# Performance work log

Measured on AMD Instinct MI355X. Metric: run time of the kernel, lower is better.

## Reference

```python
import jax, jax.numpy as jnp
import numpy as np

N_NODES = 50000
N_EDGES = 600000
IN_CH = 300
HID = 128
N_CLASSES = 2
N_GRAPHS = 128
BN_EPS = 1e-5


def setup_inputs() -> dict:
    key = jax.random.key(0)
    ks = jax.random.split(key, 24)
    x = jax.random.normal(ks[0], (N_NODES, IN_CH), dtype=jnp.float32)
    edge_index = jax.random.randint(ks[1], (2, N_EDGES), 0, N_NODES, dtype=jnp.int64)
    batch = jnp.sort(jax.random.randint(ks[2], (N_NODES,), 0, N_GRAPHS, dtype=jnp.int64))

    def glorot(k, shape):
        fan_in, fan_out = shape
        s = jnp.sqrt(2.0 / (fan_in + fan_out)).astype(jnp.float32)
        return jax.random.normal(k, shape, dtype=jnp.float32) * s

    inp = {"x": x, "edge_index": edge_index, "batch": batch}
    # SAGEConv params: W_l (neighbor branch), W_r (root branch), bias
    dims = [(IN_CH, HID), (HID, HID), (HID, HID)]
    for i, (din, dout) in enumerate(dims, start=1):
        inp[f"W{i}l"] = glorot(ks[3 * i], (din, dout))
        inp[f"W{i}r"] = glorot(ks[3 * i + 1], (din, dout))
        inp[f"b{i}"] = jnp.zeros((dout,), dtype=jnp.float32)
        inp[f"g{i}"] = jnp.ones((dout,), dtype=jnp.float32)   # BN gamma
        inp[f"be{i}"] = jnp.zeros((dout,), dtype=jnp.float32)  # BN beta
    inp["Wc"] = glorot(ks[20], (HID, N_CLASSES))
    inp["bc"] = jnp.zeros((N_CLASSES,), dtype=jnp.float32)
    return inp


def _sage_conv(x, src, dst, Wl, Wr, b):
    # mean-aggregate neighbor features (messages flow src -> dst)
    msg_sum = jax.ops.segment_sum(x[src], dst, num_segments=N_NODES)
    deg = jax.ops.segment_sum(jnp.ones((src.shape[0],), dtype=x.dtype), dst,
                              num_segments=N_NODES)
    mean = msg_sum / jnp.maximum(deg, 1.0)[:, None]
    return mean @ Wl + x @ Wr + b


def _bn_relu(h, gamma, beta):
    mu = jnp.mean(h, axis=0)
    var = jnp.var(h, axis=0)
    h = (h - mu) * jax.lax.rsqrt(var + BN_EPS) * gamma + beta
    return jax.nn.relu(h)


def reference(x, edge_index, batch,
              W1l, W1r, b1, g1, be1,
              W2l, W2r, b2, g2, be2,
              W3l, W3r, b3, g3, be3,
              Wc, bc):
    src, dst = edge_index[0], edge_index[1]
    h = _bn_relu(_sage_conv(x, src, dst, W1l, W1r, b1), g1, be1)
    h = _bn_relu(_sage_conv(h, src, dst, W2l, W2r, b2), g2, be2)
    h = _bn_relu(_sage_conv(h, src, dst, W3l, W3r, b3), g3, be3)
    # global mean pool per graph
    pooled = jax.ops.segment_sum(h, batch, num_segments=N_GRAPHS)
    cnt = jax.ops.segment_sum(jnp.ones((h.shape[0],), dtype=h.dtype), batch,
                              num_segments=N_GRAPHS)
    hg = pooled / jnp.maximum(cnt, 1.0)[:, None]
    out = hg @ Wc + bc
    return out, hg
```

## Files before the change

kernel.cpp:

```cpp
#include <hip/hip_runtime.h>

#define N_NODES   50000
#define N_EDGES   600000
#define IN_CH     300
#define HID       128
#define N_CLASSES 2
#define N_GRAPHS  128
#define BN_EPS    1e-5f

#define NB ((N_NODES + 511) / 512)
#define KP1 320
#define NREP 32
#define DEGB ((N_EDGES + 255) / 256)

typedef __attribute__((ext_vector_type(8))) short bf8_t;
typedef __attribute__((ext_vector_type(4))) float f4_t;

__device__ __forceinline__ unsigned short f2bf(float x) {
    union { float f; unsigned u; } q; q.f = x;
    unsigned r = q.u + 0x7fffu + ((q.u >> 16) & 1u);
    return (unsigned short)(r >> 16);
}
__device__ __forceinline__ float bf2f(unsigned short h) {
    union { float f; unsigned u; } q; q.u = ((unsigned)h) << 16; return q.f;
}

__global__ __launch_bounds__(256) void deg_prepw(const int* __restrict__ dst,
                                                 int* __restrict__ ideg,
                                                 const float* __restrict__ W1l,
                                                 const float* __restrict__ W1r,
                                                 const float* __restrict__ W2l,
                                                 const float* __restrict__ W2r,
                                                 const float* __restrict__ W3l,
                                                 const float* __restrict__ W3r,
                                                 unsigned short* __restrict__ B1h,
                                                 unsigned short* __restrict__ B1l,
                                                 unsigned short* __restrict__ B2h,
                                                 unsigned short* __restrict__ B2l,
                                                 unsigned short* __restrict__ B3h,
                                                 unsigned short* __restrict__ B3l) {
    int b = blockIdx.x;
    if (b < DEGB) {
        int e = b * 256 + threadIdx.x;
        if (e < N_EDGES) atomicAdd(&ideg[dst[e]], 1);
        return;
    }
    int pb = b - DEGB;
    int layer, base;
    if (pb < 320)      { layer = 0; base = pb; }
    else if (pb < 448) { layer = 1; base = pb - 320; }
    else               { layer = 2; base = pb - 448; }
    int Kp = (layer == 0) ? KP1 : HID;
    int K  = (layer == 0) ? IN_CH : HID;
    const float* Wl = (layer == 0) ? W1l : ((layer == 1) ? W2l : W3l);
    const float* Wr = (layer == 0) ? W1r : ((layer == 1) ? W2r : W3r);
    unsigned short* Bh = (layer == 0) ? B1h : ((layer == 1) ? B2h : B3h);
    unsigned short* Bl = (layer == 0) ? B1l : ((layer == 1) ? B2l : B3l);
    int idx = base * 256 + threadIdx.x;
    int n = idx / Kp;
    int k = idx - n * Kp;
    float v = 0.f;
    if (k < K) v = (n < 128) ? Wl[k * 128 + n] : Wr[k * 128 + (n - 128)];
    unsigned short h = f2bf(v);
    unsigned short l = f2bf(v - bf2f(h));
    int NST   = Kp >> 5;
    int ntile = n >> 4;
    int l16n  = n & 15;
    int kstep = k >> 5;
    int kk    = k & 31;
    int lane2 = (kk >> 3) * 16 + l16n;
    int addr  = ((ntile * NST + kstep) * 64 + lane2) * 8 + (kk & 7);
    Bh[addr] = h;
    Bl[addr] = l;
}

__global__ __launch_bounds__(256) void scan_fused(const int* __restrict__ ideg,
                                                  int* __restrict__ row_start,
                                                  float* __restrict__ invdeg,
                                                  int* __restrict__ bsum,
                                                  int* __restrict__ bflag) {
    int b = blockIdx.x, t = threadIdx.x;
    int lane = t & 63, wv = t >> 6;
    int i0 = b * 512 + t * 2;
    int v0 = 0, v1 = 0;
    if (i0 < N_NODES) {
        int2 v = *(const int2*)&ideg[i0];
        v0 = v.x; v1 = v.y;
    }
    int tot = v0 + v1;
    int s = tot;
#pragma unroll
    for (int d = 1; d < 64; d <<= 1) {
        int u = __shfl_up(s, d);
        if (lane >= d) s += u;
    }
    __shared__ int ws[4];
    if (lane == 63) ws[wv] = s;
    __syncthreads();
    int btot = ws[0] + ws[1] + ws[2] + ws[3];
    if (t == 0) {
        atomicExch(&bsum[b], btot);
        __threadfence();
        atomicExch(&bflag[b], 1);
    }
    int part = 0;
    if (t < b) {
        while (atomicAdd(&bflag[t], 0) == 0) {}
        part = atomicAdd(&bsum[t], 0);
    }
#pragma unroll
    for (int d = 1; d < 64; d <<= 1) part += __shfl_down(part, d);
    __shared__ int ps[4];
    if (lane == 0) ps[wv] = part;
    __syncthreads();
    int boff = ps[0] + ps[1] + ps[2] + ps[3];
    int woff = 0;
    for (int w = 0; w < wv; ++w) woff += ws[w];
    int base = boff + woff + (s - tot);
    if (i0 < N_NODES) {
        row_start[i0]     = base;
        row_start[i0 + 1] = base + v0;
        invdeg[i0]     = 1.0f / fmaxf((float)v0, 1.0f);
        invdeg[i0 + 1] = 1.0f / fmaxf((float)v1, 1.0f);
    }
    if (t == 0 && b == NB - 1) row_start[N_NODES] = boff + btot;
}

__global__ __launch_bounds__(256) void fill_kernel(const int* __restrict__ src,
                                                   const int* __restrict__ dst,
                                                   const int* __restrict__ row_start,
                                                   int* __restrict__ cursor,
                                                   int* __restrict__ csr_src) {
    int e = blockIdx.x * 256 + threadIdx.x;
    if (e >= N_EDGES) return;
    int d = dst[e];
    int pos = row_start[d] + atomicAdd(&cursor[d], 1);
    csr_src[pos] = src[e];
}

__global__ __launch_bounds__(256) void gemm_mfma_x(const float* __restrict__ X,
                                                   int M,
                                                   const unsigned short* __restrict__ Bhi,
                                                   const unsigned short* __restrict__ Blo,
                                                   const float* __restrict__ bias,
                                                   unsigned short* __restrict__ C0,
                                                   float* __restrict__ C1) {
    __shared__ __align__(16) unsigned short sAh[10 * 1024];
    __shared__ __align__(16) unsigned short sAl[10 * 1024];

    const int tid  = threadIdx.x;
    const int lane = tid & 63;
    const int wave = tid >> 6;
    const int l16  = lane & 15;
    const int quad = lane >> 4;
    const long m0  = (long)blockIdx.x * 32;
    const int  n0  = wave * 64;

    f4_t acc[2][4];
#pragma unroll
    for (int mt = 0; mt < 2; ++mt)
#pragma unroll
        for (int nt = 0; nt < 4; ++nt) acc[mt][nt] = (f4_t){0.f, 0.f, 0.f, 0.f};

    {
        const int ar  = tid >> 3;
        const int sub = tid & 7;
        long agr = m0 + ar;
        if (agr >= M) agr = M - 1;
        const float* gX = X + agr * IN_CH;
        const int swm = (ar >> 1) & 3;
        float4 va[5][2];
#pragma unroll
        for (int i = 0; i < 5; ++i) {
            int c  = sub + 8 * i;
            int gk = c * 8;
            va[i][0] = (gk + 4 <= IN_CH) ? *(const float4*)(gX + gk)
                                         : make_float4(0.f, 0.f, 0.f, 0.f);
            va[i][1] = (gk + 8 <= IN_CH) ? *(const float4*)(gX + gk + 4)
                                         : make_float4(0.f, 0.f, 0.f, 0.f);
        }
#pragma unroll
        for (int i = 0; i < 5; ++i) {
            int c     = sub + 8 * i;
            int kstep = c >> 2;
            int cpa   = (c & 3) ^ swm;
            float f[8];
            f[0] = va[i][0].x; f[1] = va[i][0].y; f[2] = va[i][0].z; f[3] = va[i][0].w;
            f[4] = va[i][1].x; f[5] = va[i][1].y; f[6] = va[i][1].z; f[7] = va[i][1].w;
            bf8_t h8, l8;
#pragma unroll
            for (int j = 0; j < 8; ++j) {
                unsigned short h = f2bf(f[j]);
                h8[j] = (short)h;
                l8[j] = (short)f2bf(f[j] - bf2f(h));
            }
            int idx = kstep * 1024 + ar * 32 + cpa * 8;
            *(bf8_t*)&sAh[idx] = h8;
            *(bf8_t*)&sAl[idx] = l8;
        }
    }
    __syncthreads();

    const int rsw = (quad ^ ((l16 >> 1) & 3)) * 8;
    const int NT  = KP1 / 32;
    const bf8_t* Bh0 = (const bf8_t*)Bhi;
    const bf8_t* Bl0 = (const bf8_t*)Blo;

    auto loadB = [&](int t, bf8_t (&bh)[4], bf8_t (&bl)[4]) {
#pragma unroll
        for (int nt = 0; nt < 4; ++nt) {
            long bi = ((long)(wave * 4 + nt) * NT + t) * 64 + lane;
            bh[nt] = Bh0[bi];
            bl[nt] = Bl0[bi];
        }
    };

    bf8_t bhv[4], blv[4];
    loadB(0, bhv, blv);
    for (int t = 0; t < NT; ++t) {
        bf8_t nbh[4], nbl[4];
        const bool more = (t + 1 < NT);
        if (more) loadB(t + 1, nbh, nbl);

        bf8_t ah[2], al[2];
#pragma unroll
        for (int mt = 0; mt < 2; ++mt) {
            int idx = t * 1024 + (mt * 16 + l16) * 32 + rsw;
            ah[mt] = *(const bf8_t*)&sAh[idx];
            al[mt] = *(const bf8_t*)&sAl[idx];
        }
#pragma unroll
        for (int nt = 0; nt < 4; ++nt)
#pragma unroll
            for (int mt = 0; mt < 2; ++mt)
                acc[mt][nt] = __builtin_amdgcn_mfma_f32_16x16x32_bf16(ah[mt], bhv[nt], acc[mt][nt], 0, 0, 0);
#pragma unroll
        for (int nt = 0; nt < 4; ++nt)
#pragma unroll
            for (int mt = 0; mt < 2; ++mt)
                acc[mt][nt] = __builtin_amdgcn_mfma_f32_16x16x32_bf16(al[mt], bhv[nt], acc[mt][nt], 0, 0, 0);
#pragma unroll
        for (int nt = 0; nt < 4; ++nt)
#pragma unroll
            for (int mt = 0; mt < 2; ++mt)
                acc[mt][nt] = __builtin_amdgcn_mfma_f32_16x16x32_bf16(ah[mt], blv[nt], acc[mt][nt], 0, 0, 0);

        if (more) {
#pragma unroll
            for (int nt = 0; nt < 4; ++nt) {
                bhv[nt] = nbh[nt];
                blv[nt] = nbl[nt];
            }
        }
    }

    const bool left = (n0 < 128);
    if (left) {
        int ncol[4];
#pragma unroll
        for (int nt = 0; nt < 4; ++nt) ncol[nt] = n0 + nt * 16 + l16;
#pragma unroll
        for (int mt = 0; mt < 2; ++mt)
#pragma unroll
            for (int r = 0; r < 4; ++r) {
                long row = m0 + mt * 16 + quad * 4 + r;
                if (row < M) {
#pragma unroll
                    for (int nt = 0; nt < 4; ++nt)
                        C0[row * 128 + ncol[nt]] = f2bf(acc[mt][nt][r]);
                }
            }
    } else {
        float badd[4];
        int   ncol[4];
#pragma unroll
        for (int nt = 0; nt < 4; ++nt) {
            int ng = n0 + nt * 16 + l16 - 128;
            ncol[nt] = ng;
            badd[nt] = bias[ng];
        }
#pragma unroll
        for (int mt = 0; mt < 2; ++mt)
#pragma unroll
            for (int r = 0; r < 4; ++r) {
                long row = m0 + mt * 16 + quad * 4 + r;
                if (row < M) {
#pragma unroll
                    for (int nt = 0; nt < 4; ++nt)
                        C1[row * 128 + ncol[nt]] = acc[mt][nt][r] + badd[nt];
                }
            }
    }
}

__global__ __launch_bounds__(256) void gemm_mfma_h(const float* __restrict__ Hpre,
                                                   int M,
                                                   const float* __restrict__ rep,
                                                   const float* __restrict__ gamma,
                                                   const float* __restrict__ beta,
                                                   const unsigned short* __restrict__ Bhi,
                                                   const unsigned short* __restrict__ Blo,
                                                   const float* __restrict__ bias,
                                                   unsigned short* __restrict__ C0,
                                                   float* __restrict__ C1) {
    __shared__ __align__(16) unsigned short sAh[4 * 2048];
    __shared__ __align__(16) unsigned short sAl[4 * 2048];
    __shared__ float sSC[256];

    const int tid  = threadIdx.x;
    const int lane = tid & 63;
    const int wave = tid >> 6;
    const int l16  = lane & 15;
    const int quad = lane >> 4;
    const long m0  = (long)blockIdx.x * 64;
    const int  n0  = wave * 64;

    {
        float* S = (float*)sAh;
        float a = 0.f;
#pragma unroll
        for (int r = 0; r < NREP; ++r) a += rep[r * 256 + tid];
        S[tid] = a;
        __syncthreads();
        if (tid < HID) {
            const float invn = 1.0f / (float)N_NODES;
            float mu  = S[tid] * invn;
            float var = S[HID + tid] * invn - mu * mu;
            float sc  = gamma[tid] * rsqrtf(var + BN_EPS);
            sSC[tid]       = sc;
            sSC[HID + tid] = beta[tid] - mu * sc;
        }
        __syncthreads();
    }

    f4_t acc[4][4];
#pragma unroll
    for (int mt = 0; mt < 4; ++mt)
#pragma unroll
        for (int nt = 0; nt < 4; ++nt) acc[mt][nt] = (f4_t){0.f, 0.f, 0.f, 0.f};

    {
        const int ar = tid >> 2;
        const int cl = tid & 3;
        long agr = m0 + ar;
        if (agr >= M) agr = M - 1;
        const float* gH = Hpre + agr * HID;
        const int swm = (ar >> 1) & 3;
        float4 va[4][2];
#pragma unroll
        for (int i = 0; i < 4; ++i) {
            int gk = (cl + 4 * i) * 8;
            va[i][0] = *(const float4*)(gH + gk);
            va[i][1] = *(const float4*)(gH + gk + 4);
        }
#pragma unroll
        for (int i = 0; i < 4; ++i) {
            int c     = cl + 4 * i;
            int kstep = c >> 2;
            int cpa   = (c & 3) ^ swm;
            int gk    = c * 8;
            float4 s0 = *(const float4*)&sSC[gk];
            float4 s1 = *(const float4*)&sSC[gk + 4];
            float4 t0 = *(const float4*)&sSC[HID + gk];
            float4 t1 = *(const float4*)&sSC[HID + gk + 4];
            float f[8];
            f[0] = fmaxf(va[i][0].x * s0.x + t0.x, 0.f);
            f[1] = fmaxf(va[i][0].y * s0.y + t0.y, 0.f);
            f[2] = fmaxf(va[i][0].z * s0.z + t0.z, 0.f);
            f[3] = fmaxf(va[i][0].w * s0.w + t0.w, 0.f);
            f[4] = fmaxf(va[i][1].x * s1.x + t1.x, 0.f);
            f[5] = fmaxf(va[i][1].y * s1.y + t1.y, 0.f);
            f[6] = fmaxf(va[i][1].z * s1.z + t1.z, 0.f);
            f[7] = fmaxf(va[i][1].w * s1.w + t1.w, 0.f);
            bf8_t h8, l8;
#pragma unroll
            for (int j = 0; j < 8; ++j) {
                unsigned short h = f2bf(f[j]);
                h8[j] = (short)h;
                l8[j] = (short)f2bf(f[j] - bf2f(h));
            }
            int idx = kstep * 2048 + ar * 32 + cpa * 8;
            *(bf8_t*)&sAh[idx] = h8;
            *(bf8_t*)&sAl[idx] = l8;
        }
    }
    __syncthreads();

    const int rsw = (quad ^ ((l16 >> 1) & 3)) * 8;
    const int NT  = HID / 32;
    const bf8_t* Bh0 = (const bf8_t*)Bhi;
    const bf8_t* Bl0 = (const bf8_t*)Blo;

    auto loadB = [&](int t, bf8_t (&bh)[4], bf8_t (&bl)[4]) {
#pragma unroll
        for (int nt = 0; nt < 4; ++nt) {
            long bi = ((long)(wave * 4 + nt) * NT + t) * 64 + lane;
            bh[nt] = Bh0[bi];
            bl[nt] = Bl0[bi];
        }
    };

    bf8_t bhv[4], blv[4];
    loadB(0, bhv, blv);
#pragma unroll
    for (int t = 0; t < 4; ++t) {
        bf8_t nbh[4], nbl[4];
        const bool more = (t < 3);
        if (more) loadB(t + 1, nbh, nbl);

        bf8_t ah[4], al[4];
#pragma unroll
        for (int mt = 0; mt < 4; ++mt) {
            int idx = t * 2048 + (mt * 16 + l16) * 32 + rsw;
            ah[mt] = *(const bf8_t*)&sAh[idx];
            al[mt] = *(const bf8_t*)&sAl[idx];
        }
#pragma unroll
        for (int nt = 0; nt < 4; ++nt)
#pragma unroll
            for (int mt = 0; mt < 4; ++mt)
                acc[mt][nt] = __builtin_amdgcn_mfma_f32_16x16x32_bf16(ah[mt], bhv[nt], acc[mt][nt], 0, 0, 0);
#pragma unroll
        for (int nt = 0; nt < 4; ++nt)
#pragma unroll
            for (int mt = 0; mt < 4; ++mt)
                acc[mt][nt] = __builtin_amdgcn_mfma_f32_16x16x32_bf16(al[mt], bhv[nt], acc[mt][nt], 0, 0, 0);
#pragma unroll
        for (int nt = 0; nt < 4; ++nt)
#pragma unroll
            for (int mt = 0; mt < 4; ++mt)
                acc[mt][nt] = __builtin_amdgcn_mfma_f32_16x16x32_bf16(ah[mt], blv[nt], acc[mt][nt], 0, 0, 0);

        if (more) {
#pragma unroll
            for (int nt = 0; nt < 4; ++nt) {
                bhv[nt] = nbh[nt];
                blv[nt] = nbl[nt];
            }
        }
    }

    const bool left = (n0 < 128);
    if (left) {
        int ncol[4];
#pragma unroll
        for (int nt = 0; nt < 4; ++nt) ncol[nt] = n0 + nt * 16 + l16;
#pragma unroll
        for (int mt = 0; mt < 4; ++mt)
#pragma unroll
            for (int r = 0; r < 4; ++r) {
                long row = m0 + mt * 16 + quad * 4 + r;
                if (row < M) {
#pragma unroll
                    for (int nt = 0; nt < 4; ++nt)
                        C0[row * 128 + ncol[nt]] = f2bf(acc[mt][nt][r]);
                }
            }
    } else {
        float badd[4];
        int   ncol[4];
#pragma unroll
        for (int nt = 0; nt < 4; ++nt) {
            int ng = n0 + nt * 16 + l16 - 128;
            ncol[nt] = ng;
            badd[nt] = bias[ng];
        }
#pragma unroll
        for (int mt = 0; mt < 4; ++mt)
#pragma unroll
            for (int r = 0; r < 4; ++r) {
                long row = m0 + mt * 16 + quad * 4 + r;
                if (row < M) {
#pragma unroll
                    for (int nt = 0; nt < 4; ++nt)
                        C1[row * 128 + ncol[nt]] = acc[mt][nt][r] + badd[nt];
                }
            }
    }
}

__global__ __launch_bounds__(256) void gather_agg(const unsigned short* __restrict__ Pl,
                                                  const int* __restrict__ row_start,
                                                  const int* __restrict__ csr_src,
                                                  const float* __restrict__ invdeg,
                                                  float* __restrict__ out,
                                                  float* __restrict__ rep) {
    int slot = threadIdx.x >> 5;
    int lane = threadIdx.x & 31;
    int node = blockIdx.x * 8 + slot;
    int beg = row_start[node];
    int end = row_start[node + 1];
    const unsigned short* base = Pl + lane * 4;
    float sx = 0.f, sy = 0.f, sz = 0.f, sw = 0.f;
    int j = beg;
    int deg = end - beg;

    if (deg > 0) {
        int n16 = (deg < 16) ? deg : 16;
        int idx[16];
#pragma unroll
        for (int u = 0; u < 16; ++u)
            idx[u] = csr_src[(u < n16) ? (j + u) : j];
        ushort4 v[16];
#pragma unroll
        for (int u = 0; u < 16; ++u)
            v[u] = *(const ushort4*)(base + (long)idx[u] * HID);
#pragma unroll
        for (int u = 0; u < 16; ++u) {
            float m = (u < n16) ? 1.f : 0.f;
            sx += m * bf2f(v[u].x); sy += m * bf2f(v[u].y);
            sz += m * bf2f(v[u].z); sw += m * bf2f(v[u].w);
        }
        j += n16;
    }
    for (; j + 8 <= end; j += 8) {
        int idx[8];
#pragma unroll
        for (int u = 0; u < 8; ++u) idx[u] = csr_src[j + u];
        ushort4 v[8];
#pragma unroll
        for (int u = 0; u < 8; ++u) v[u] = *(const ushort4*)(base + (long)idx[u] * HID);
#pragma unroll
        for (int u = 0; u < 8; ++u) {
            sx += bf2f(v[u].x); sy += bf2f(v[u].y);
            sz += bf2f(v[u].z); sw += bf2f(v[u].w);
        }
    }
    if (j + 4 <= end) {
        int idx[4];
#pragma unroll
        for (int u = 0; u < 4; ++u) idx[u] = csr_src[j + u];
        ushort4 v[4];
#pragma unroll
        for (int u = 0; u < 4; ++u) v[u] = *(const ushort4*)(base + (long)idx[u] * HID);
#pragma unroll
        for (int u = 0; u < 4; ++u) {
            sx += bf2f(v[u].x); sy += bf2f(v[u].y);
            sz += bf2f(v[u].z); sw += bf2f(v[u].w);
        }
        j += 4;
    }
    for (; j < end; ++j) {
        int i0 = csr_src[j];
        ushort4 v0 = *(const ushort4*)(base + (long)i0 * HID);
        sx += bf2f(v0.x); sy += bf2f(v0.y); sz += bf2f(v0.z); sw += bf2f(v0.w);
    }
    float w = invdeg[node];
    float* o = out + (long)node * HID + lane * 4;
    float4 cur = *(float4*)o;
    cur.x += sx * w;
    cur.y += sy * w;
    cur.z += sz * w;
    cur.w += sw * w;
    *(float4*)o = cur;

    __shared__ float red[8][HID];
    float* repb = rep + (blockIdx.x & (NREP - 1)) * 256;
    *(float4*)&red[slot][lane * 4] = make_float4(cur.x, cur.y, cur.z, cur.w);
    __syncthreads();
    if (threadIdx.x < HID) {
        float tsum = 0.f;
#pragma unroll
        for (int s = 0; s < 8; ++s) tsum += red[s][threadIdx.x];
        atomicAdd(&repb[threadIdx.x], tsum);
    }
    __syncthreads();
    *(float4*)&red[slot][lane * 4] = make_float4(cur.x * cur.x, cur.y * cur.y,
                                                 cur.z * cur.z, cur.w * cur.w);
    __syncthreads();
    if (threadIdx.x < HID) {
        float tsum = 0.f;
#pragma unroll
        for (int s = 0; s < 8; ++s) tsum += red[s][threadIdx.x];
        atomicAdd(&repb[HID + threadIdx.x], tsum);
    }
}

__global__ __launch_bounds__(1024) void poolhead_bn(const float* __restrict__ h,
                                                    const int* __restrict__ batch,
                                                    const float* __restrict__ rep,
                                                    const float* __restrict__ gamma,
                                                    const float* __restrict__ beta,
                                                    const float* __restrict__ Wc,
                                                    const float* __restrict__ bc,
                                                    float* __restrict__ out) {
    __shared__ float S[256];
    __shared__ float SC[256];
    int g = blockIdx.x;
    int t = threadIdx.x;
    int c = t & 127;
    int half = t >> 7;
    if (t < 256) {
        float a = 0.f;
#pragma unroll
        for (int r = 0; r < NREP; ++r) a += rep[r * 256 + t];
        S[t] = a;
    }
    __shared__ int lo_sh, hi_sh;
    if (t == 0) {
        int lo = 0, hi = N_NODES;
        while (lo < hi) { int m = (lo + hi) >> 1; if (batch[m] < g) lo = m + 1; else hi = m; }
        lo_sh = lo;
        int lo2 = lo, hi2 = N_NODES;
        while (lo2 < hi2) { int m = (lo2 + hi2) >> 1; if (batch[m] < g + 1) lo2 = m + 1; else hi2 = m; }
        hi_sh = lo2;
    }
    __syncthreads();
    if (t < HID) {
        const float invn = 1.0f / (float)N_NODES;
        float mu  = S[t] * invn;
        float var = S[HID + t] * invn - mu * mu;
        float sc  = gamma[t] * rsqrtf(var + BN_EPS);
        SC[t]       = sc;
        SC[HID + t] = beta[t] - mu * sc;
    }
    __syncthreads();
    float bsc = SC[c], bsh = SC[HID + c];
    int lo = lo_sh, hi = hi_sh;
    float a0 = 0.f, a1 = 0.f, a2 = 0.f, a3 = 0.f;
    int r = lo + half;
    for (; r + 24 < hi; r += 32) {
        a0 += fmaxf(h[(long)(r +  0) * HID + c] * bsc + bsh, 0.f);
        a1 += fmaxf(h[(long)(r +  8) * HID + c] * bsc + bsh, 0.f);
        a2 += fmaxf(h[(long)(r + 16) * HID + c] * bsc + bsh, 0.f);
        a3 += fmaxf(h[(long)(r + 24) * HID + c] * bsc + bsh, 0.f);
    }
    for (; r < hi; r += 8) a0 += fmaxf(h[(long)r * HID + c] * bsc + bsh, 0.f);
    __shared__ float red[8][HID];
    red[half][c] = (a0 + a1) + (a2 + a3);
    __syncthreads();
    __shared__ float r0[HID], r1[HID];
    if (t < HID) {
        float inv = 1.0f / fmaxf((float)(hi - lo), 1.0f);
        float v = 0.f;
#pragma unroll
        for (int s = 0; s < 8; ++s) v += red[s][t];
        v *= inv;
        out[N_GRAPHS * N_CLASSES + g * HID + t] = v;
        r0[t] = v * Wc[t * 2 + 0];
        r1[t] = v * Wc[t * 2 + 1];
    }
    __syncthreads();
    if (t < 2) {
        const float* rr = t ? r1 : r0;
        float sum = bc[t];
        for (int i = 0; i < HID; ++i) sum += rr[i];
        out[g * 2 + t] = sum;
    }
}

extern "C" void kernel_launch(void* const* d_in, const int* in_sizes, int n_in,
                              void* d_out, int out_size, void* d_ws, size_t ws_size,
                              hipStream_t stream) {
    const float* x     = (const float*)d_in[0];
    const int*   ei    = (const int*)d_in[1];
    const int*   batch = (const int*)d_in[2];
    const float* W1l = (const float*)d_in[3];
    const float* W1r = (const float*)d_in[4];
    const float* b1  = (const float*)d_in[5];
    const float* g1  = (const float*)d_in[6];
    const float* be1 = (const float*)d_in[7];
    const float* W2l = (const float*)d_in[8];
    const float* W2r = (const float*)d_in[9];
    const float* b2  = (const float*)d_in[10];
    const float* g2  = (const float*)d_in[11];
    const float* be2 = (const float*)d_in[12];
    const float* W3l = (const float*)d_in[13];
    const float* W3r = (const float*)d_in[14];
    const float* b3  = (const float*)d_in[15];
    const float* g3  = (const float*)d_in[16];
    const float* be3 = (const float*)d_in[17];
    const float* Wc  = (const float*)d_in[18];
    const float* bc  = (const float*)d_in[19];

    const int* src = ei;
    const int* dst = ei + N_EDGES;

    float* ws = (float*)d_ws;
    const long FEAT = (long)N_NODES * HID;
    unsigned short* Pl16 = (unsigned short*)ws;
    float* buf1 = ws + FEAT;
    float* buf2 = ws + 2 * FEAT;
    int*   ideg      = (int*)(ws + 3 * FEAT);
    int*   cursor    = ideg + N_NODES;
    int*   bsum      = cursor + N_NODES;
    int*   bflag     = bsum + 128;
    int*   row_start = bflag + 128;
    int*   csr_src   = row_start + N_NODES + 4;
    float* invdeg    = (float*)(csr_src + N_EDGES);
    float* reps      = invdeg + N_NODES;
    unsigned short* B1h = (unsigned short*)(reps + 3 * NREP * 256);
    unsigned short* B1l = B1h + 256 * KP1;
    unsigned short* B2h = B1l + 256 * KP1;
    unsigned short* B2l = B2h + 256 * HID;
    unsigned short* B3h = B2l + 256 * HID;
    unsigned short* B3l = B3h + 256 * HID;

    float* outp = (float*)d_out;

    const int gemmx_grid  = (N_NODES + 31) / 32;
    const int gemmh_grid  = (N_NODES + 63) / 64;
    const int gather_grid = N_NODES / 8;
    const int dp_grid     = DEGB + 320 + 128 + 128;

    hipMemsetAsync(ideg, 0, (2 * N_NODES + 256) * sizeof(int), stream);
    hipMemsetAsync(reps, 0, 3 * NREP * 256 * sizeof(float), stream);

    deg_prepw<<<dp_grid, 256, 0, stream>>>(dst, ideg, W1l, W1r, W2l, W2r, W3l, W3r,
                                           B1h, B1l, B2h, B2l, B3h, B3l);
    scan_fused<<<NB, 256, 0, stream>>>(ideg, row_start, invdeg, bsum, bflag);
    fill_kernel<<<(N_EDGES + 255) / 256, 256, 0, stream>>>(src, dst, row_start, cursor, csr_src);

    gemm_mfma_x<<<gemmx_grid, 256, 0, stream>>>(x, N_NODES, B1h, B1l, b1, Pl16, buf1);
    gather_agg<<<gather_grid, 256, 0, stream>>>(Pl16, row_start, csr_src, invdeg, buf1, reps);

    gemm_mfma_h<<<gemmh_grid, 256, 0, stream>>>(buf1, N_NODES, reps, g1, be1,
                                                B2h, B2l, b2, Pl16, buf2);
    gather_agg<<<gather_grid, 256, 0, stream>>>(Pl16, row_start, csr_src, invdeg, buf2, reps + NREP * 256);

    gemm_mfma_h<<<gemmh_grid, 256, 0, stream>>>(buf2, N_NODES, reps + NREP * 256, g2, be2,
                                                B3h, B3l, b3, Pl16, buf1);
    gather_agg<<<gather_grid, 256, 0, stream>>>(Pl16, row_start, csr_src, invdeg, buf1, reps + 2 * NREP * 256);

    poolhead_bn<<<N_GRAPHS, 1024, 0, stream>>>(buf1, batch, reps + 2 * NREP * 256,
                                               g3, be3, Wc, bc, outp);
}
```

Before: 374.4 us.

## Enlarge first-layer GEMM tile and hoist BN scale/shift into tiny prep kernel

The first-layer GEMM now covers 64 rows per block instead of 32, so each B fragment load feeds twice as many MFMAs and the grid is halved, at the cost of more LDS and accumulator registers. The BN statistics reduction, previously repeated in every GEMM block and every pool block, moves into a single-block bn_prep kernel that writes scale/shift to global memory, which the consumers then read directly. The gather kernel also merges its sum and sum-of-squares reductions into one shared-memory pass, removing a barrier round. The trade is three extra tiny kernel launches.

```diff
diff --git a/kernel.cpp b/kernel.cpp
--- a/kernel.cpp
+++ b/kernel.cpp
@@ -138,6 +138,27 @@
     csr_src[pos] = src[e];
 }
 
+__global__ __launch_bounds__(256) void bn_prep(const float* __restrict__ rep,
+                                               const float* __restrict__ gamma,
+                                               const float* __restrict__ beta,
+                                               float* __restrict__ SCg) {
+    __shared__ float S[256];
+    int t = threadIdx.x;
+    float a = 0.f;
+#pragma unroll
+    for (int r = 0; r < NREP; ++r) a += rep[r * 256 + t];
+    S[t] = a;
+    __syncthreads();
+    if (t < HID) {
+        const float invn = 1.0f / (float)N_NODES;
+        float mu  = S[t] * invn;
+        float var = S[HID + t] * invn - mu * mu;
+        float sc  = gamma[t] * rsqrtf(var + BN_EPS);
+        SCg[t]       = sc;
+        SCg[HID + t] = beta[t] - mu * sc;
+    }
+}
+
 __global__ __launch_bounds__(256) void gemm_mfma_x(const float* __restrict__ X,
                                                    int M,
                                                    const unsigned short* __restrict__ Bhi,
@@ -145,58 +166,61 @@
                                                    const float* __restrict__ bias,
                                                    unsigned short* __restrict__ C0,
                                                    float* __restrict__ C1) {
-    __shared__ __align__(16) unsigned short sAh[10 * 1024];
-    __shared__ __align__(16) unsigned short sAl[10 * 1024];
+    __shared__ __align__(16) unsigned short sAh[10 * 2048];
+    __shared__ __align__(16) unsigned short sAl[10 * 2048];
 
     const int tid  = threadIdx.x;
     const int lane = tid & 63;
     const int wave = tid >> 6;
     const int l16  = lane & 15;
     const int quad = lane >> 4;
-    const long m0  = (long)blockIdx.x * 32;
+    const long m0  = (long)blockIdx.x * 64;
     const int  n0  = wave * 64;
 
-    f4_t acc[2][4];
-#pragma unroll
-    for (int mt = 0; mt < 2; ++mt)
+    f4_t acc[4][4];
+#pragma unroll
+    for (int mt = 0; mt < 4; ++mt)
 #pragma unroll
         for (int nt = 0; nt < 4; ++nt) acc[mt][nt] = (f4_t){0.f, 0.f, 0.f, 0.f};
 
     {
-        const int ar  = tid >> 3;
-        const int sub = tid & 7;
+        const int ar  = tid >> 2;
+        const int sub = tid & 3;
         long agr = m0 + ar;
         if (agr >= M) agr = M - 1;
         const float* gX = X + agr * IN_CH;
         const int swm = (ar >> 1) & 3;
-        float4 va[5][2];
-#pragma unroll
-        for (int i = 0; i < 5; ++i) {
-            int c  = sub + 8 * i;
-            int gk = c * 8;
-            va[i][0] = (gk + 4 <= IN_CH) ? *(const float4*)(gX + gk)
-                                         : make_float4(0.f, 0.f, 0.f, 0.f);
-            va[i][1] = (gk + 8 <= IN_CH) ? *(const float4*)(gX + gk + 4)
-                                         : make_float4(0.f, 0.f, 0.f, 0.f);
-        }
-#pragma unroll
-        for (int i = 0; i < 5; ++i) {
-            int c     = sub + 8 * i;
-            int kstep = c >> 2;
-            int cpa   = (c & 3) ^ swm;
-            float f[8];
-            f[0] = va[i][0].x; f[1] = va[i][0].y; f[2] = va[i][0].z; f[3] = va[i][0].w;
-            f[4] = va[i][1].x; f[5] = va[i][1].y; f[6] = va[i][1].z; f[7] = va[i][1].w;
-            bf8_t h8, l8;
-#pragma unroll
-            for (int j = 0; j < 8; ++j) {
-                unsigned short h = f2bf(f[j]);
-                h8[j] = (short)h;
-                l8[j] = (short)f2bf(f[j] - bf2f(h));
-            }
-            int idx = kstep * 1024 + ar * 32 + cpa * 8;
-            *(bf8_t*)&sAh[idx] = h8;
-            *(bf8_t*)&sAl[idx] = l8;
+        const int cpa = sub ^ swm;
+#pragma unroll
+        for (int bt = 0; bt < 2; ++bt) {
+            float4 va[5][2];
+#pragma unroll
+            for (int i = 0; i < 5; ++i) {
+                int c  = sub + 4 * (bt * 5 + i);
+                int gk = c * 8;
+                va[i][0] = (gk + 4 <= IN_CH) ? *(const float4*)(gX + gk)
+                                             : make_float4(0.f, 0.f, 0.f, 0.f);
+                va[i][1] = (gk + 8 <= IN_CH) ? *(const float4*)(gX + gk + 4)
+                                             : make_float4(0.f, 0.f, 0.f, 0.f);
+            }
+#pragma unroll
+            for (int i = 0; i < 5; ++i) {
+                int c     = sub + 4 * (bt * 5 + i);
+                int kstep = c >> 2;
+                float f[8];
+                f[0] = va[i][0].x; f[1] = va[i][0].y; f[2] = va[i][0].z; f[3] = va[i][0].w;
+                f[4] = va[i][1].x; f[5] = va[i][1].y; f[6] = va[i][1].z; f[7] = va[i][1].w;
+                bf8_t h8, l8;
+#pragma unroll
+                for (int j = 0; j < 8; ++j) {
+                    unsigned short h = f2bf(f[j]);
+                    h8[j] = (short)h;
+                    l8[j] = (short)f2bf(f[j] - bf2f(h));
+                }
+                int idx = kstep * 2048 + ar * 32 + cpa * 8;
+                *(bf8_t*)&sAh[idx] = h8;
+                *(bf8_t*)&sAl[idx] = l8;
+            }
         }
     }
     __syncthreads();
@@ -222,27 +246,27 @@
         const bool more = (t + 1 < NT);
         if (more) loadB(t + 1, nbh, nbl);
 
-        bf8_t ah[2], al[2];
-#pragma unroll
-        for (int mt = 0; mt < 2; ++mt) {
-            int idx = t * 1024 + (mt * 16 + l16) * 32 + rsw;
+        bf8_t ah[4], al[4];
+#pragma unroll
+        for (int mt = 0; mt < 4; ++mt) {
+            int idx = t * 2048 + (mt * 16 + l16) * 32 + rsw;
             ah[mt] = *(const bf8_t*)&sAh[idx];
             al[mt] = *(const bf8_t*)&sAl[idx];
         }
 #pragma unroll
         for (int nt = 0; nt < 4; ++nt)
 #pragma unroll
-            for (int mt = 0; mt < 2; ++mt)
+            for (int mt = 0; mt < 4; ++mt)
                 acc[mt][nt] = __builtin_amdgcn_mfma_f32_16x16x32_bf16(ah[mt], bhv[nt], acc[mt][nt], 0, 0, 0);
 #pragma unroll
         for (int nt = 0; nt < 4; ++nt)
 #pragma unroll
-            for (int mt = 0; mt < 2; ++mt)
+            for (int mt = 0; mt < 4; ++mt)
                 acc[mt][nt] = __builtin_amdgcn_mfma_f32_16x16x32_bf16(al[mt], bhv[nt], acc[mt][nt], 0, 0, 0);
 #pragma unroll
         for (int nt = 0; nt < 4; ++nt)
 #pragma unroll
-            for (int mt = 0; mt < 2; ++mt)
+            for (int mt = 0; mt < 4; ++mt)
                 acc[mt][nt] = __builtin_amdgcn_mfma_f32_16x16x32_bf16(ah[mt], blv[nt], acc[mt][nt], 0, 0, 0);
 
         if (more) {
@@ -260,7 +284,7 @@
 #pragma unroll
         for (int nt = 0; nt < 4; ++nt) ncol[nt] = n0 + nt * 16 + l16;
 #pragma unroll
-        for (int mt = 0; mt < 2; ++mt)
+        for (int mt = 0; mt < 4; ++mt)
 #pragma unroll
             for (int r = 0; r < 4; ++r) {
                 long row = m0 + mt * 16 + quad * 4 + r;
@@ -280,7 +304,7 @@
             badd[nt] = bias[ng];
         }
 #pragma unroll
-        for (int mt = 0; mt < 2; ++mt)
+        for (int mt = 0; mt < 4; ++mt)
 #pragma unroll
             for (int r = 0; r < 4; ++r) {
                 long row = m0 + mt * 16 + quad * 4 + r;
@@ -295,9 +319,7 @@
 
 __global__ __launch_bounds__(256) void gemm_mfma_h(const float* __restrict__ Hpre,
                                                    int M,
-                                                   const float* __restrict__ rep,
-                                                   const float* __restrict__ gamma,
-                                                   const float* __restrict__ beta,
+                                                   const float* __restrict__ SCg,
                                                    const unsigned short* __restrict__ Bhi,
                                                    const unsigned short* __restrict__ Blo,
                                                    const float* __restrict__ bias,
@@ -305,7 +327,6 @@
                                                    float* __restrict__ C1) {
     __shared__ __align__(16) unsigned short sAh[4 * 2048];
     __shared__ __align__(16) unsigned short sAl[4 * 2048];
-    __shared__ float sSC[256];
 
     const int tid  = threadIdx.x;
     const int lane = tid & 63;
@@ -315,24 +336,6 @@
     const long m0  = (long)blockIdx.x * 64;
     const int  n0  = wave * 64;
 
-    {
-        float* S = (float*)sAh;
-        float a = 0.f;
-#pragma unroll
-        for (int r = 0; r < NREP; ++r) a += rep[r * 256 + tid];
-        S[tid] = a;
-        __syncthreads();
-        if (tid < HID) {
-            const float invn = 1.0f / (float)N_NODES;
-            float mu  = S[tid] * invn;
-            float var = S[HID + tid] * invn - mu * mu;
-            float sc  = gamma[tid] * rsqrtf(var + BN_EPS);
-            sSC[tid]       = sc;
-            sSC[HID + tid] = beta[tid] - mu * sc;
-        }
-        __syncthreads();
-    }
-
     f4_t acc[4][4];
 #pragma unroll
     for (int mt = 0; mt < 4; ++mt)
@@ -346,6 +349,7 @@
         if (agr >= M) agr = M - 1;
         const float* gH = Hpre + agr * HID;
         const int swm = (ar >> 1) & 3;
+        const int cpa = cl ^ swm;
         float4 va[4][2];
 #pragma unroll
         for (int i = 0; i < 4; ++i) {
@@ -357,12 +361,11 @@
         for (int i = 0; i < 4; ++i) {
             int c     = cl + 4 * i;
             int kstep = c >> 2;
-            int cpa   = (c & 3) ^ swm;
             int gk    = c * 8;
-            float4 s0 = *(const float4*)&sSC[gk];
-            float4 s1 = *(const float4*)&sSC[gk + 4];
-            float4 t0 = *(const float4*)&sSC[HID + gk];
-            float4 t1 = *(const float4*)&sSC[HID + gk + 4];
+            float4 s0 = *(const float4*)&SCg[gk];
+            float4 s1 = *(const float4*)&SCg[gk + 4];
+            float4 t0 = *(const float4*)&SCg[HID + gk];
+            float4 t1 = *(const float4*)&SCg[HID + gk + 4];
             float f[8];
             f[0] = fmaxf(va[i][0].x * s0.x + t0.x, 0.f);
             f[1] = fmaxf(va[i][0].y * s0.y + t0.y, 0.f);
@@ -559,43 +562,30 @@
     *(float4*)&red[slot][lane * 4] = make_float4(cur.x, cur.y, cur.z, cur.w);
     __syncthreads();
     if (threadIdx.x < HID) {
-        float tsum = 0.f;
-#pragma unroll
-        for (int s = 0; s < 8; ++s) tsum += red[s][threadIdx.x];
+        float tsum = 0.f, tsq = 0.f;
+#pragma unroll
+        for (int s = 0; s < 8; ++s) {
+            float v = red[s][threadIdx.x];
+            tsum += v;
+            tsq  += v * v;
+        }
         atomicAdd(&repb[threadIdx.x], tsum);
-    }
-    __syncthreads();
-    *(float4*)&red[slot][lane * 4] = make_float4(cur.x * cur.x, cur.y * cur.y,
-                                                 cur.z * cur.z, cur.w * cur.w);
-    __syncthreads();
-    if (threadIdx.x < HID) {
-        float tsum = 0.f;
-#pragma unroll
-        for (int s = 0; s < 8; ++s) tsum += red[s][threadIdx.x];
-        atomicAdd(&repb[HID + threadIdx.x], tsum);
+        atomicAdd(&repb[HID + threadIdx.x], tsq);
     }
 }
 
 __global__ __launch_bounds__(1024) void poolhead_bn(const float* __restrict__ h,
                                                     const int* __restrict__ batch,
-                                                    const float* __restrict__ rep,
-                                                    const float* __restrict__ gamma,
-                                                    const float* __restrict__ beta,
+                                                    const float* __restrict__ SCg,
                                                     const float* __restrict__ Wc,
                                                     const float* __restrict__ bc,
                                                     float* __restrict__ out) {
-    __shared__ float S[256];
     __shared__ float SC[256];
     int g = blockIdx.x;
     int t = threadIdx.x;
     int c = t & 127;
     int half = t >> 7;
-    if (t < 256) {
-        float a = 0.f;
-#pragma unroll
-        for (int r = 0; r < NREP; ++r) a += rep[r * 256 + t];
-        S[t] = a;
-    }
+    if (t < 256) SC[t] = SCg[t];
     __shared__ int lo_sh, hi_sh;
     if (t == 0) {
         int lo = 0, hi = N_NODES;
@@ -604,15 +594,6 @@
         int lo2 = lo, hi2 = N_NODES;
         while (lo2 < hi2) { int m = (lo2 + hi2) >> 1; if (batch[m] < g + 1) lo2 = m + 1; else hi2 = m; }
         hi_sh = lo2;
-    }
-    __syncthreads();
-    if (t < HID) {
-        const float invn = 1.0f / (float)N_NODES;
-        float mu  = S[t] * invn;
-        float var = S[HID + t] * invn - mu * mu;
-        float sc  = gamma[t] * rsqrtf(var + BN_EPS);
-        SC[t]       = sc;
-        SC[HID + t] = beta[t] - mu * sc;
     }
     __syncthreads();
     float bsc = SC[c], bsh = SC[HID + c];
@@ -689,7 +670,10 @@
     int*   csr_src   = row_start + N_NODES + 4;
     float* invdeg    = (float*)(csr_src + N_EDGES);
     float* reps      = invdeg + N_NODES;
-    unsigned short* B1h = (unsigned short*)(reps + 3 * NREP * 256);
+    float* SC1g      = reps + 3 * NREP * 256;
+    float* SC2g      = SC1g + 256;
+    float* SC3g      = SC2g + 256;
+    unsigned short* B1h = (unsigned short*)(SC3g + 256);
     unsigned short* B1l = B1h + 256 * KP1;
     unsigned short* B2h = B1l + 256 * KP1;
     unsigned short* B2l = B2h + 256 * HID;
@@ -698,8 +682,7 @@
 
     float* outp = (float*)d_out;
 
-    const int gemmx_grid  = (N_NODES + 31) / 32;
-    const int gemmh_grid  = (N_NODES + 63) / 64;
+    const int gemm_grid   = (N_NODES + 63) / 64;
     const int gather_grid = N_NODES / 8;
     const int dp_grid     = DEGB + 320 + 128 + 128;
 
@@ -711,17 +694,19 @@
     scan_fused<<<NB, 256, 0, stream>>>(ideg, row_start, invdeg, bsum, bflag);
     fill_kernel<<<(N_EDGES + 255) / 256, 256, 0, stream>>>(src, dst, row_start, cursor, csr_src);
 
-    gemm_mfma_x<<<gemmx_grid, 256, 0, stream>>>(x, N_NODES, B1h, B1l, b1, Pl16, buf1);
+    gemm_mfma_x<<<gemm_grid, 256, 0, stream>>>(x, N_NODES, B1h, B1l, b1, Pl16, buf1);
     gather_agg<<<gather_grid, 256, 0, stream>>>(Pl16, row_start, csr_src, invdeg, buf1, reps);
-
-    gemm_mfma_h<<<gemmh_grid, 256, 0, stream>>>(buf1, N_NODES, reps, g1, be1,
-                                                B2h, B2l, b2, Pl16, buf2);
+    bn_prep<<<1, 256, 0, stream>>>(reps, g1, be1, SC1g);
+
+    gemm_mfma_h<<<gemm_grid, 256, 0, stream>>>(buf1, N_NODES, SC1g,
+                                               B2h, B2l, b2, Pl16, buf2);
     gather_agg<<<gather_grid, 256, 0, stream>>>(Pl16, row_start, csr_src, invdeg, buf2, reps + NREP * 256);
-
-    gemm_mfma_h<<<gemmh_grid, 256, 0, stream>>>(buf2, N_NODES, reps + NREP * 256, g2, be2,
-                                                B3h, B3l, b3, Pl16, buf1);
+    bn_prep<<<1, 256, 0, stream>>>(reps + NREP * 256, g2, be2, SC2g);
+
+    gemm_mfma_h<<<gemm_grid, 256, 0, stream>>>(buf2, N_NODES, SC2g,
+                                               B3h, B3l, b3, Pl16, buf1);
     gather_agg<<<gather_grid, 256, 0, stream>>>(Pl16, row_start, csr_src, invdeg, buf1, reps + 2 * NREP * 256);
-
-    poolhead_bn<<<N_GRAPHS, 1024, 0, stream>>>(buf1, batch, reps + 2 * NREP * 256,
-                                               g3, be3, Wc, bc, outp);
-}
+    bn_prep<<<1, 256, 0, stream>>>(reps + 2 * NREP * 256, g3, be3, SC3g);
+
+    poolhead_bn<<<N_GRAPHS, 1024, 0, stream>>>(buf1, batch, SC3g, Wc, bc, outp);
+}
```

Measured after the change: 379.2 us. About the same (+1.3%).
